# Kernel optimization log

Measured on AMD Instinct MI355X. Metric: run time of the kernel, lower is better.

Reference implementation:

```python
import jax, jax.numpy as jnp
import numpy as np

NUM_LEVELS = 4
RADIUS = 3


def bilinear_sample(feat, coords):
    """feat: (B,H,W,C); coords: (B, ..., 2) with [x,y] order. Returns (B, ..., C).
    Matches the original: corner indices are clipped FIRST, then weights are
    computed from the clipped indices."""
    B, H, W, C = feat.shape
    x = coords[..., 0]
    y = coords[..., 1]
    x0 = jnp.clip(jnp.floor(x).astype(jnp.int32), 0, W - 1)
    x1 = jnp.clip(jnp.floor(x).astype(jnp.int32) + 1, 0, W - 1)
    y0 = jnp.clip(jnp.floor(y).astype(jnp.int32), 0, H - 1)
    y1 = jnp.clip(jnp.floor(y).astype(jnp.int32) + 1, 0, H - 1)
    x0f = x0.astype(jnp.float32); x1f = x1.astype(jnp.float32)
    y0f = y0.astype(jnp.float32); y1f = y1.astype(jnp.float32)
    wa = (x1f - x) * (y1f - y)
    wb = (x1f - x) * (y - y0f)
    wc = (x - x0f) * (y1f - y)
    wd = (x - x0f) * (y - y0f)
    bidx = jnp.arange(B).reshape((B,) + (1,) * (coords.ndim - 2))
    Ia = feat[bidx, y0, x0]
    Ib = feat[bidx, y1, x0]
    Ic = feat[bidx, y0, x1]
    Id = feat[bidx, y1, x1]
    return wa[..., None] * Ia + wb[..., None] * Ib + wc[..., None] * Ic + wd[..., None] * Id


def _normalize(v):
    return v / (jnp.linalg.norm(v, axis=-1, keepdims=True) + 1e-06)


def setup_inputs() -> dict:
    key = jax.random.key(0)
    k1, k2, k3, k4 = jax.random.split(key, 4)
    B, H, W, C, N = 2, 64, 64, 256, 4096
    fmap1 = jax.random.normal(k1, (B, H, W, C), dtype=jnp.float32)
    fmap2 = jax.random.normal(k2, (B, H, W, C), dtype=jnp.float32)
    scale = jnp.array([W - 1, H - 1], dtype=jnp.float32)
    coords1 = jax.random.uniform(k3, (B, N, 2), dtype=jnp.float32) * scale
    coords2 = jax.random.uniform(k4, (B, N, 2), dtype=jnp.float32) * scale
    return {"fmap1": fmap1, "fmap2": fmap2, "coords1": coords1, "coords2": coords2}


def reference(fmap1, fmap2, coords1, coords2):
    r = RADIUS
    B, H, W, C = fmap1.shape
    feat1 = _normalize(bilinear_sample(fmap1, coords1))  # (B,N,C)
    # Offset grid, dy-major then dx (matches the original nested loops),
    # stored as [dx, dy] to match `coords + [dx, dy]`.
    d = jnp.arange(-r, r + 1, dtype=jnp.float32)
    dyg, dxg = jnp.meshgrid(d, d, indexing='ij')
    offs = jnp.stack([dxg.ravel(), dyg.ravel()], axis=-1)  # (K,2), K=(2r+1)^2
    corr_list = []
    fmap2_l = fmap2  # cascaded pyramid, as in the original
    for level in range(NUM_LEVELS):
        if level > 0:
            fmap2_l = jax.image.resize(
                fmap2_l, (B, H // 2 ** level, W // 2 ** level, C), method='bilinear')
        H_l, W_l = fmap2_l.shape[1], fmap2_l.shape[2]
        f2n = _normalize(fmap2_l)
        scale = 2.0 ** level
        c = coords2[:, :, None, :] / scale + offs[None, None, :, :]  # (B,N,K,2)
        c = jnp.clip(c, jnp.zeros(2, jnp.float32),
                     jnp.array([W_l - 1, H_l - 1], dtype=jnp.float32))
        feat2 = bilinear_sample(f2n, c)  # (B,N,K,C)
        corr_list.append(jnp.einsum('bnc,bnkc->bnk', feat1, feat2))
    return jnp.concatenate(corr_list, axis=-1)  # (B,N,NUM_LEVELS*K)
```

## Files before the change

### kernel.cpp

```cpp
#include <hip/hip_runtime.h>
#include <math.h>

#define NB   2
#define H0   64
#define W0   64
#define NC   256
#define NPTS 4096
#define NLVL 4
#define NK   49

__device__ __forceinline__ float wave_reduce_sum(float v) {
    for (int m = 32; m >= 1; m >>= 1)
        v += __shfl_xor(v, m, 64);
    return v;
}

__device__ __forceinline__ float wave_reduce_max(float v) {
    for (int m = 32; m >= 1; m >>= 1)
        v = fmaxf(v, __shfl_xor(v, m, 64));
    return v;
}

__device__ __forceinline__ int dot4i(unsigned a, unsigned b, int c) {
#if defined(__has_builtin)
#if __has_builtin(__builtin_amdgcn_sdot4)
    return __builtin_amdgcn_sdot4((int)a, (int)b, c, false);
#else
    c += (((int)(a << 24)) >> 24) * (((int)(b << 24)) >> 24);
    c += (((int)(a << 16)) >> 24) * (((int)(b << 16)) >> 24);
    c += (((int)(a <<  8)) >> 24) * (((int)(b <<  8)) >> 24);
    c += (((int)a) >> 24)         * (((int)b) >> 24);
    return c;
#endif
#else
    c += (((int)(a << 24)) >> 24) * (((int)(b << 24)) >> 24);
    c += (((int)(a << 16)) >> 24) * (((int)(b << 16)) >> 24);
    c += (((int)(a <<  8)) >> 24) * (((int)(b <<  8)) >> 24);
    c += (((int)a) >> 24)         * (((int)b) >> 24);
    return c;
#endif
}

__device__ __forceinline__ void quant_store(float nx, float ny, float nz, float nw,
                                            unsigned char* __restrict__ qout,
                                            size_t pixIdx,
                                            float* __restrict__ sout, int lane) {
    float m = fmaxf(fmaxf(fabsf(nx), fabsf(ny)), fmaxf(fabsf(nz), fabsf(nw)));
    float M = wave_reduce_max(m);
    float s = (M > 0.f) ? 127.f / M : 0.f;
    int qx = __float2int_rn(nx * s), qy = __float2int_rn(ny * s);
    int qz = __float2int_rn(nz * s), qw = __float2int_rn(nw * s);
    unsigned p = (qx & 0xff) | ((qy & 0xff) << 8) | ((qz & 0xff) << 16) | ((qw & 0xff) << 24);
    ((unsigned*)(qout + pixIdx * NC))[lane] = p;
    if (lane == 0) sout[pixIdx] = (M > 0.f) ? M / 127.f : 0.f;
}

__device__ __forceinline__ void down_norm(const float* __restrict__ in,
                                          float* __restrict__ raw_out,
                                          unsigned char* __restrict__ qout,
                                          float* __restrict__ sout,
                                          int Hi, int Wi, int wid, int lane) {
    int Ho = Hi >> 1, Wo = Wi >> 1;
    int b = wid / (Ho * Wo);
    int rem = wid - b * (Ho * Wo);
    int yo = rem / Wo, xo = rem - yo * Wo;
    float wy[4], wx[4]; int ty[4], tx[4];
    float sy = 0.f, sx = 0.f;
    for (int j = 0; j < 4; ++j) {
        float w = (j == 0 || j == 3) ? 1.f : 3.f;
        int yi = 2 * yo - 1 + j;
        float wyj = (yi >= 0 && yi < Hi) ? w : 0.f;
        ty[j] = min(max(yi, 0), Hi - 1); wy[j] = wyj; sy += wyj;
        int xi = 2 * xo - 1 + j;
        float wxj = (xi >= 0 && xi < Wi) ? w : 0.f;
        tx[j] = min(max(xi, 0), Wi - 1); wx[j] = wxj; sx += wxj;
    }
    float inv_s = 1.f / (sy * sx);
    float ax = 0.f, ay = 0.f, az = 0.f, aw = 0.f;
    const float4* basep = (const float4*)(in + (size_t)b * Hi * Wi * NC);
    for (int jy = 0; jy < 4; ++jy) {
        if (wy[jy] == 0.f) continue;
        for (int jx = 0; jx < 4; ++jx) {
            float w = wy[jy] * wx[jx];
            if (w == 0.f) continue;
            float4 v = basep[(ty[jy] * Wi + tx[jx]) * (NC / 4) + lane];
            ax += w * v.x; ay += w * v.y; az += w * v.z; aw += w * v.w;
        }
    }
    ax *= inv_s; ay *= inv_s; az *= inv_s; aw *= inv_s;
    float ss = wave_reduce_sum(ax * ax + ay * ay + az * az + aw * aw);
    float inv = 1.f / (sqrtf(ss) + 1e-6f);
    size_t po = (size_t)b * Ho * Wo + (size_t)yo * Wo + xo;
    if (raw_out) {
        float4 r; r.x = ax; r.y = ay; r.z = az; r.w = aw;
        ((float4*)raw_out)[po * (NC / 4) + lane] = r;
    }
    quant_store(ax * inv, ay * inv, az * inv, aw * inv, qout, po, sout, lane);
}

__global__ __launch_bounds__(256)
void pre_kernel(const float* __restrict__ fmap1,
                const float* __restrict__ fmap2,
                const float* __restrict__ coords1,
                unsigned char* __restrict__ f1q, float* __restrict__ fsc,
                unsigned char* __restrict__ q0,  float* __restrict__ s0,
                float* __restrict__ raw1,
                unsigned char* __restrict__ q1,  float* __restrict__ s1) {
    int blk  = blockIdx.x;
    int wv   = threadIdx.x >> 6;
    int lane = threadIdx.x & 63;
    if (blk < 2048) {
        int pt = blk * 4 + wv;
        int b = pt / NPTS;
        float x = coords1[pt * 2 + 0];
        float y = coords1[pt * 2 + 1];
        int x0 = min(max((int)floorf(x), 0), W0 - 1);
        int y0 = min(max((int)floorf(y), 0), H0 - 1);
        int x1 = min(x0 + 1, W0 - 1);
        int y1 = min(y0 + 1, H0 - 1);
        float wxh = x - (float)x0, wxl = (float)x1 - x;
        float wyh = y - (float)y0, wyl = (float)y1 - y;
        float wa = wxl * wyl, wb = wxl * wyh, wc = wxh * wyl, wd = wxh * wyh;
        const float4* base = (const float4*)(fmap1 + (size_t)b * H0 * W0 * NC);
        float4 Ia = base[(y0 * W0 + x0) * (NC / 4) + lane];
        float4 Ib = base[(y1 * W0 + x0) * (NC / 4) + lane];
        float4 Ic = base[(y0 * W0 + x1) * (NC / 4) + lane];
        float4 Id = base[(y1 * W0 + x1) * (NC / 4) + lane];
        float vx = wa * Ia.x + wb * Ib.x + wc * Ic.x + wd * Id.x;
        float vy = wa * Ia.y + wb * Ib.y + wc * Ic.y + wd * Id.y;
        float vz = wa * Ia.z + wb * Ib.z + wc * Ic.z + wd * Id.z;
        float vw = wa * Ia.w + wb * Ib.w + wc * Ic.w + wd * Id.w;
        float ss = wave_reduce_sum(vx * vx + vy * vy + vz * vz + vw * vw);
        float inv = 1.0f / (sqrtf(ss) + 1e-6f);
        quant_store(vx * inv, vy * inv, vz * inv, vw * inv, f1q, pt, fsc, lane);
    } else if (blk < 4096) {
        int p = (blk - 2048) * 4 + wv;
        float4 v = ((const float4*)fmap2)[(size_t)p * (NC / 4) + lane];
        float ss = wave_reduce_sum(v.x * v.x + v.y * v.y + v.z * v.z + v.w * v.w);
        float inv = 1.0f / (sqrtf(ss) + 1e-6f);
        quant_store(v.x * inv, v.y * inv, v.z * inv, v.w * inv, q0, p, s0, lane);
    } else {
        int wid = (blk - 4096) * 4 + wv;
        down_norm(fmap2, raw1, q1, s1, H0, W0, wid, lane);
    }
}

__global__ __launch_bounds__(256)
void small_kernel(const float* __restrict__ raw1,
                  unsigned char* __restrict__ q2, float* __restrict__ s2,
                  unsigned char* __restrict__ q3, float* __restrict__ s3) {
    __shared__ float4 part[4][64];
    int blk  = blockIdx.x;
    int wv   = threadIdx.x >> 6;
    int lane = threadIdx.x & 63;
    float ax = 0.f, ay = 0.f, az = 0.f, aw = 0.f;
    unsigned char* qout; float* sout; size_t po;

    if (blk < 512) {
        int b = blk >> 8, rem = blk & 255;
        int yo = rem >> 4, xo = rem & 15;
        float wy[4], wx[4]; int ty[4], tx[4];
        float sy = 0.f, sx = 0.f;
#pragma unroll
        for (int j = 0; j < 4; ++j) {
            float w = (j == 0 || j == 3) ? 1.f : 3.f;
            int yi = 2 * yo - 1 + j;
            float wyj = (yi >= 0 && yi < 32) ? w : 0.f;
            ty[j] = min(max(yi, 0), 31); wy[j] = wyj; sy += wyj;
            int xi = 2 * xo - 1 + j;
            float wxj = (xi >= 0 && xi < 32) ? w : 0.f;
            tx[j] = min(max(xi, 0), 31); wx[j] = wxj; sx += wxj;
        }
        float inv_s = 1.f / (sy * sx);
        const float4* basep = (const float4*)(raw1 + (size_t)b * 32 * 32 * NC);
        int jy = wv;
        if (wy[jy] != 0.f) {
#pragma unroll
            for (int jx = 0; jx < 4; ++jx) {
                float w = wy[jy] * wx[jx] * inv_s;
                if (wx[jx] == 0.f) continue;
                float4 v = basep[(ty[jy] * 32 + tx[jx]) * (NC / 4) + lane];
                ax += w * v.x; ay += w * v.y; az += w * v.z; aw += w * v.w;
            }
        }
        qout = q2; sout = s2; po = (size_t)b * 256 + yo * 16 + xo;
    } else {
        int wid = blk - 512;
        int b = wid >> 6, rem = wid & 63;
        int yo = rem >> 3, xo = rem & 7;
        float Wt[2][10]; int base[2];
        for (int d = 0; d < 2; ++d) {
            int o = d ? xo : yo;
            base[d] = 4 * o - 3;
            float W[10];
            for (int k = 0; k < 10; ++k) W[k] = 0.f;
            float S2 = 0.f;
            for (int j = 0; j < 4; ++j) {
                int yj = 2 * o - 1 + j;
                if (yj < 0 || yj >= 16) continue;
                float wj = (j == 0 || j == 3) ? 1.f : 3.f;
                S2 += wj;
                int yi0 = 2 * yj - 1;
                float wi[4], s1v = 0.f;
                for (int i2 = 0; i2 < 4; ++i2) {
                    int yi = yi0 + i2;
                    wi[i2] = (yi >= 0 && yi < 32) ? ((i2 == 0 || i2 == 3) ? 1.f : 3.f) : 0.f;
                    s1v += wi[i2];
                }
                float sc = wj / s1v;
                for (int i2 = 0; i2 < 4; ++i2)
                    if (wi[i2] > 0.f) W[yi0 + i2 - base[d]] += wi[i2] * sc;
            }
            float invS = 1.f / S2;
            for (int k = 0; k < 10; ++k) Wt[d][k] = W[k] * invS;
        }
        const float4* basep = (const float4*)(raw1 + (size_t)b * 32 * 32 * NC);
        for (int ky = wv; ky < 10; ky += 4) {
            float wyk = Wt[0][ky];
            if (wyk == 0.f) continue;
            int yi = base[0] + ky;
#pragma unroll
            for (int kx = 0; kx < 10; ++kx) {
                float wxk = Wt[1][kx];
                if (wxk == 0.f) continue;
                int xi = base[1] + kx;
                float wgt = wyk * wxk;
                float4 v = basep[(yi * 32 + xi) * (NC / 4) + lane];
                ax += wgt * v.x; ay += wgt * v.y; az += wgt * v.z; aw += wgt * v.w;
            }
        }
        qout = q3; sout = s3; po = (size_t)b * 64 + yo * 8 + xo;
    }

    float4 pr; pr.x = ax; pr.y = ay; pr.z = az; pr.w = aw;
    part[wv][lane] = pr;
    __syncthreads();
    if (wv == 0) {
        float4 p0 = part[0][lane], p1 = part[1][lane];
        float4 p2 = part[2][lane], p3 = part[3][lane];
        ax = p0.x + p1.x + p2.x + p3.x;
        ay = p0.y + p1.y + p2.y + p3.y;
        az = p0.z + p1.z + p2.z + p3.z;
        aw = p0.w + p1.w + p2.w + p3.w;
        float ss = wave_reduce_sum(ax * ax + ay * ay + az * az + aw * aw);
        float inv = 1.f / (sqrtf(ss) + 1e-6f);
        quant_store(ax * inv, ay * inv, az * inv, aw * inv, qout, po, sout, lane);
    }
}

__device__ __forceinline__ int tile_dot(const uint4* buf, const uint4* a4) {
    int ac = 0;
#pragma unroll
    for (int s = 0; s < 4; ++s) {
        uint4 u = buf[s], av = a4[s];
        ac = dot4i(av.x, u.x, ac);
        ac = dot4i(av.y, u.y, ac);
        ac = dot4i(av.z, u.z, ac);
        ac = dot4i(av.w, u.w, ac);
    }
    return ac;
}

__global__ __launch_bounds__(256)
void corr_kernel(const unsigned char* __restrict__ f1q,
                 const float* __restrict__ fsc,
                 const float* __restrict__ coords2,
                 const unsigned char* __restrict__ q0, const float* __restrict__ s0,
                 const unsigned char* __restrict__ q1, const float* __restrict__ s1,
                 const unsigned char* __restrict__ q2, const float* __restrict__ s2,
                 const unsigned char* __restrict__ q3, const float* __restrict__ s3,
                 float* __restrict__ out) {
    __shared__ float Ds[NLVL][64];
    int pt = blockIdx.x;
    int b  = pt / NPTS;
    int t  = threadIdx.x;

    int w    = t >> 6;
    int lane = t & 63;
    int Wl = W0 >> w, Hl = H0 >> w;
    float invs = 1.0f / (float)(1 << w);
    float cx = coords2[pt * 2 + 0] * invs;
    float cy = coords2[pt * 2 + 1] * invs;
    int ix = (int)floorf(cx), iy = (int)floorf(cy);

    const unsigned char* f2q = (w == 0) ? q0 : (w == 1) ? q1 : (w == 2) ? q2 : q3;
    const float*         f2s = (w == 0) ? s0 : (w == 1) ? s1 : (w == 2) ? s2 : s3;

    int cg = lane & 3;
    int pq = lane >> 2;

    const uint4* pixp[4];
    int pidx[4];
#pragma unroll
    for (int i = 0; i < 4; ++i) {
        int p  = i * 16 + pq;
        int jx = p & 7, jy = p >> 3;
        int px = min(max(ix - 3 + jx, 0), Wl - 1);
        int py = min(max(iy - 3 + jy, 0), Hl - 1);
        pidx[i] = (b * Hl + py) * Wl + px;
        pixp[i] = (const uint4*)(f2q + (size_t)pidx[i] * NC);
    }

    uint4 bufs[4][4];
#pragma unroll
    for (int i = 0; i < 4; ++i)
#pragma unroll
        for (int s = 0; s < 4; ++s)
            bufs[i][s] = pixp[i][s * 4 + cg];

    const uint4* f1p = (const uint4*)(f1q + (size_t)pt * NC);
    uint4 a4[4];
#pragma unroll
    for (int s = 0; s < 4; ++s) a4[s] = f1p[s * 4 + cg];

    float sb[4];
#pragma unroll
    for (int i = 0; i < 4; ++i) sb[i] = f2s[pidx[i]];
    float sa = fsc[pt];

#pragma unroll
    for (int i = 0; i < 4; ++i) {
        int r = tile_dot(bufs[i], a4);
        r += __shfl_xor(r, 1, 64);
        r += __shfl_xor(r, 2, 64);
        if (cg == 0) Ds[w][i * 16 + pq] = (float)r * sa * sb[i];
    }
    __syncthreads();

    if (lane < NK) {
        int tyk = lane / 7, txk = lane % 7;
        float dx = (float)(txk - 3), dy = (float)(tyk - 3);
        float x = fminf(fmaxf(cx + dx, 0.f), (float)(Wl - 1));
        float y = fminf(fmaxf(cy + dy, 0.f), (float)(Hl - 1));
        int x0 = (int)floorf(x);
        int y0 = (int)floorf(y);
        int x1 = min(x0 + 1, Wl - 1);
        int y1 = min(y0 + 1, Hl - 1);
        float wxh = x - (float)x0, wxl = (float)x1 - x;
        float wyh = y - (float)y0, wyl = (float)y1 - y;
        int sx0 = min(max(x0 - ix + 3, 0), 7);
        int sx1 = min(max(x1 - ix + 3, 0), 7);
        int sy0 = min(max(y0 - iy + 3, 0), 7);
        int sy1 = min(max(y1 - iy + 3, 0), 7);
        float v = wxl * wyl * Ds[w][sy0 * 8 + sx0]
                + wxl * wyh * Ds[w][sy1 * 8 + sx0]
                + wxh * wyl * Ds[w][sy0 * 8 + sx1]
                + wxh * wyh * Ds[w][sy1 * 8 + sx1];
        out[(size_t)pt * (NLVL * NK) + w * NK + lane] = v;
    }
}

extern "C" void kernel_launch(void* const* d_in, const int* in_sizes, int n_in,
                              void* d_out, int out_size, void* d_ws, size_t ws_size,
                              hipStream_t stream) {
    const float* fmap1   = (const float*)d_in[0];
    const float* fmap2   = (const float*)d_in[1];
    const float* coords1 = (const float*)d_in[2];
    const float* coords2 = (const float*)d_in[3];
    float* out = (float*)d_out;
    float* ws  = (float*)d_ws;

    float*         raw1 = ws;
    unsigned char* f1q  = (unsigned char*)(ws + 524288);
    float*         fsc  = ws + 1048576;
    unsigned char* q0   = (unsigned char*)(ws + 1056768);
    float*         s0   = ws + 1581056;
    unsigned char* q1   = (unsigned char*)(ws + 1589248);
    float*         s1   = ws + 1720320;
    unsigned char* q2   = (unsigned char*)(ws + 1722368);
    float*         s2   = ws + 1755136;
    unsigned char* q3   = (unsigned char*)(ws + 1755648);
    float*         s3   = ws + 1763840;

    pre_kernel<<<4608, 256, 0, stream>>>(fmap1, fmap2, coords1,
                                         f1q, fsc, q0, s0, raw1, q1, s1);
    small_kernel<<<640, 256, 0, stream>>>(raw1, q2, s2, q3, s3);
    corr_kernel<<<NB * NPTS, 256, 0, stream>>>(f1q, fsc, coords2,
                                               q0, s0, q1, s1, q2, s2, q3, s3, out);
}
```

Measured before the change: 109.6 us.

## Fuse pyramid build into one kernel by composing cascaded downsample weights

Removes the separate small_kernel launch and the full-precision level-1 intermediate buffer. Levels 2 and 3 are now computed straight from fmap2, using per-axis filter weights built by composing the cascaded 2x bilinear downsamples. This saves one launch and the write/read round trip of the raw level-1 map. In exchange, level-2/3 outputs read much wider footprints from the full-resolution map (up to about 22x22 pixels), and the weight arrays are dynamically indexed, which may spill to scratch. It also drops a block-wide barrier in corr_kernel, relying on each wave reading only its own shared slice.

```diff
diff --git a/kernel.cpp b/kernel.cpp
--- a/kernel.cpp
+++ b/kernel.cpp
@@ -56,7 +56,6 @@
 }
 
 __device__ __forceinline__ void down_norm(const float* __restrict__ in,
-                                          float* __restrict__ raw_out,
                                           unsigned char* __restrict__ qout,
                                           float* __restrict__ sout,
                                           int Hi, int Wi, int wid, int lane) {
@@ -91,21 +90,52 @@
     float ss = wave_reduce_sum(ax * ax + ay * ay + az * az + aw * aw);
     float inv = 1.f / (sqrtf(ss) + 1e-6f);
     size_t po = (size_t)b * Ho * Wo + (size_t)yo * Wo + xo;
-    if (raw_out) {
-        float4 r; r.x = ax; r.y = ay; r.z = az; r.w = aw;
-        ((float4*)raw_out)[po * (NC / 4) + lane] = r;
-    }
     quant_store(ax * inv, ay * inv, az * inv, aw * inv, qout, po, sout, lane);
 }
 
+__device__ void compose_axis(int o, int nst, float* W, int* pb0, int* pn) {
+    float a[22];
+    int ba = o, na = 1, ra = 64 >> nst;
+    a[0] = 1.f;
+    for (int s = 0; s < nst; ++s) {
+        float bt[22];
+        int rb = ra << 1;
+        int bb = 2 * ba - 1;
+        int nb = 2 * na + 2;
+        for (int k = 0; k < nb; ++k) bt[k] = 0.f;
+        for (int k = 0; k < na; ++k) {
+            float ak = a[k];
+            if (ak == 0.f) continue;
+            int j  = ba + k;
+            int i0 = 2 * j - 1;
+            float w0 = (i0     >= 0 && i0     < rb) ? 1.f : 0.f;
+            float w1 = (i0 + 1 >= 0 && i0 + 1 < rb) ? 3.f : 0.f;
+            float w2 = (i0 + 2 >= 0 && i0 + 2 < rb) ? 3.f : 0.f;
+            float w3 = (i0 + 3 >= 0 && i0 + 3 < rb) ? 1.f : 0.f;
+            float inv = ak / (w0 + w1 + w2 + w3);
+            int off = i0 - bb;
+            bt[off]     += w0 * inv;
+            bt[off + 1] += w1 * inv;
+            bt[off + 2] += w2 * inv;
+            bt[off + 3] += w3 * inv;
+        }
+        ba = bb; na = nb; ra = rb;
+        for (int k = 0; k < na; ++k) a[k] = bt[k];
+    }
+    *pb0 = ba; *pn = na;
+    for (int k = 0; k < na; ++k) W[k] = a[k];
+}
+
 __global__ __launch_bounds__(256)
-void pre_kernel(const float* __restrict__ fmap1,
-                const float* __restrict__ fmap2,
-                const float* __restrict__ coords1,
-                unsigned char* __restrict__ f1q, float* __restrict__ fsc,
-                unsigned char* __restrict__ q0,  float* __restrict__ s0,
-                float* __restrict__ raw1,
-                unsigned char* __restrict__ q1,  float* __restrict__ s1) {
+void build_kernel(const float* __restrict__ fmap1,
+                  const float* __restrict__ fmap2,
+                  const float* __restrict__ coords1,
+                  unsigned char* __restrict__ f1q, float* __restrict__ fsc,
+                  unsigned char* __restrict__ q0,  float* __restrict__ s0,
+                  unsigned char* __restrict__ q1,  float* __restrict__ s1,
+                  unsigned char* __restrict__ q2,  float* __restrict__ s2,
+                  unsigned char* __restrict__ q3,  float* __restrict__ s3) {
+    __shared__ float4 part[4][64];
     int blk  = blockIdx.x;
     int wv   = threadIdx.x >> 6;
     int lane = threadIdx.x & 63;
@@ -139,112 +169,55 @@
         float ss = wave_reduce_sum(v.x * v.x + v.y * v.y + v.z * v.z + v.w * v.w);
         float inv = 1.0f / (sqrtf(ss) + 1e-6f);
         quant_store(v.x * inv, v.y * inv, v.z * inv, v.w * inv, q0, p, s0, lane);
+    } else if (blk < 4608) {
+        int wid = (blk - 4096) * 4 + wv;
+        down_norm(fmap2, q1, s1, H0, W0, wid, lane);
     } else {
-        int wid = (blk - 4096) * 4 + wv;
-        down_norm(fmap2, raw1, q1, s1, H0, W0, wid, lane);
-    }
-}
-
-__global__ __launch_bounds__(256)
-void small_kernel(const float* __restrict__ raw1,
-                  unsigned char* __restrict__ q2, float* __restrict__ s2,
-                  unsigned char* __restrict__ q3, float* __restrict__ s3) {
-    __shared__ float4 part[4][64];
-    int blk  = blockIdx.x;
-    int wv   = threadIdx.x >> 6;
-    int lane = threadIdx.x & 63;
-    float ax = 0.f, ay = 0.f, az = 0.f, aw = 0.f;
-    unsigned char* qout; float* sout; size_t po;
-
-    if (blk < 512) {
-        int b = blk >> 8, rem = blk & 255;
-        int yo = rem >> 4, xo = rem & 15;
-        float wy[4], wx[4]; int ty[4], tx[4];
-        float sy = 0.f, sx = 0.f;
-#pragma unroll
-        for (int j = 0; j < 4; ++j) {
-            float w = (j == 0 || j == 3) ? 1.f : 3.f;
-            int yi = 2 * yo - 1 + j;
-            float wyj = (yi >= 0 && yi < 32) ? w : 0.f;
-            ty[j] = min(max(yi, 0), 31); wy[j] = wyj; sy += wyj;
-            int xi = 2 * xo - 1 + j;
-            float wxj = (xi >= 0 && xi < 32) ? w : 0.f;
-            tx[j] = min(max(xi, 0), 31); wx[j] = wxj; sx += wxj;
-        }
-        float inv_s = 1.f / (sy * sx);
-        const float4* basep = (const float4*)(raw1 + (size_t)b * 32 * 32 * NC);
-        int jy = wv;
-        if (wy[jy] != 0.f) {
-#pragma unroll
-            for (int jx = 0; jx < 4; ++jx) {
-                float w = wy[jy] * wx[jx] * inv_s;
-                if (wx[jx] == 0.f) continue;
-                float4 v = basep[(ty[jy] * 32 + tx[jx]) * (NC / 4) + lane];
+        int id = blk - 4608;
+        int b, yo, xo, nst;
+        unsigned char* qout; float* sout; size_t po;
+        if (id < 512) {
+            nst = 2;
+            b = id >> 8; int rem = id & 255; yo = rem >> 4; xo = rem & 15;
+            qout = q2; sout = s2; po = (size_t)b * 256 + yo * 16 + xo;
+        } else {
+            int id3 = id - 512;
+            nst = 3;
+            b = id3 >> 6; int rem = id3 & 63; yo = rem >> 3; xo = rem & 7;
+            qout = q3; sout = s3; po = (size_t)b * 64 + yo * 8 + xo;
+        }
+        float Wy[22], Wx[22];
+        int by, bx, ny, nx;
+        compose_axis(yo, nst, Wy, &by, &ny);
+        compose_axis(xo, nst, Wx, &bx, &nx);
+        const float4* basep = (const float4*)(fmap2 + (size_t)b * H0 * W0 * NC);
+        float ax = 0.f, ay = 0.f, az = 0.f, aw = 0.f;
+        for (int ky = wv; ky < ny; ky += 4) {
+            float wyk = Wy[ky];
+            if (wyk == 0.f) continue;
+            int yi = by + ky;
+            for (int kx = 0; kx < nx; ++kx) {
+                float wxk = Wx[kx];
+                if (wxk == 0.f) continue;
+                float w = wyk * wxk;
+                float4 v = basep[(yi * W0 + bx + kx) * (NC / 4) + lane];
                 ax += w * v.x; ay += w * v.y; az += w * v.z; aw += w * v.w;
             }
         }
-        qout = q2; sout = s2; po = (size_t)b * 256 + yo * 16 + xo;
-    } else {
-        int wid = blk - 512;
-        int b = wid >> 6, rem = wid & 63;
-        int yo = rem >> 3, xo = rem & 7;
-        float Wt[2][10]; int base[2];
-        for (int d = 0; d < 2; ++d) {
-            int o = d ? xo : yo;
-            base[d] = 4 * o - 3;
-            float W[10];
-            for (int k = 0; k < 10; ++k) W[k] = 0.f;
-            float S2 = 0.f;
-            for (int j = 0; j < 4; ++j) {
-                int yj = 2 * o - 1 + j;
-                if (yj < 0 || yj >= 16) continue;
-                float wj = (j == 0 || j == 3) ? 1.f : 3.f;
-                S2 += wj;
-                int yi0 = 2 * yj - 1;
-                float wi[4], s1v = 0.f;
-                for (int i2 = 0; i2 < 4; ++i2) {
-                    int yi = yi0 + i2;
-                    wi[i2] = (yi >= 0 && yi < 32) ? ((i2 == 0 || i2 == 3) ? 1.f : 3.f) : 0.f;
-                    s1v += wi[i2];
-                }
-                float sc = wj / s1v;
-                for (int i2 = 0; i2 < 4; ++i2)
-                    if (wi[i2] > 0.f) W[yi0 + i2 - base[d]] += wi[i2] * sc;
-            }
-            float invS = 1.f / S2;
-            for (int k = 0; k < 10; ++k) Wt[d][k] = W[k] * invS;
-        }
-        const float4* basep = (const float4*)(raw1 + (size_t)b * 32 * 32 * NC);
-        for (int ky = wv; ky < 10; ky += 4) {
-            float wyk = Wt[0][ky];
-            if (wyk == 0.f) continue;
-            int yi = base[0] + ky;
-#pragma unroll
-            for (int kx = 0; kx < 10; ++kx) {
-                float wxk = Wt[1][kx];
-                if (wxk == 0.f) continue;
-                int xi = base[1] + kx;
-                float wgt = wyk * wxk;
-                float4 v = basep[(yi * 32 + xi) * (NC / 4) + lane];
-                ax += wgt * v.x; ay += wgt * v.y; az += wgt * v.z; aw += wgt * v.w;
-            }
-        }
-        qout = q3; sout = s3; po = (size_t)b * 64 + yo * 8 + xo;
-    }
-
-    float4 pr; pr.x = ax; pr.y = ay; pr.z = az; pr.w = aw;
-    part[wv][lane] = pr;
-    __syncthreads();
-    if (wv == 0) {
-        float4 p0 = part[0][lane], p1 = part[1][lane];
-        float4 p2 = part[2][lane], p3 = part[3][lane];
-        ax = p0.x + p1.x + p2.x + p3.x;
-        ay = p0.y + p1.y + p2.y + p3.y;
-        az = p0.z + p1.z + p2.z + p3.z;
-        aw = p0.w + p1.w + p2.w + p3.w;
-        float ss = wave_reduce_sum(ax * ax + ay * ay + az * az + aw * aw);
-        float inv = 1.f / (sqrtf(ss) + 1e-6f);
-        quant_store(ax * inv, ay * inv, az * inv, aw * inv, qout, po, sout, lane);
+        float4 pr; pr.x = ax; pr.y = ay; pr.z = az; pr.w = aw;
+        part[wv][lane] = pr;
+        __syncthreads();
+        if (wv == 0) {
+            float4 p0 = part[0][lane], p1 = part[1][lane];
+            float4 p2 = part[2][lane], p3 = part[3][lane];
+            ax = p0.x + p1.x + p2.x + p3.x;
+            ay = p0.y + p1.y + p2.y + p3.y;
+            az = p0.z + p1.z + p2.z + p3.z;
+            aw = p0.w + p1.w + p2.w + p3.w;
+            float ss = wave_reduce_sum(ax * ax + ay * ay + az * az + aw * aw);
+            float inv = 1.f / (sqrtf(ss) + 1e-6f);
+            quant_store(ax * inv, ay * inv, az * inv, aw * inv, qout, po, sout, lane);
+        }
     }
 }
 
@@ -325,7 +298,6 @@
         r += __shfl_xor(r, 2, 64);
         if (cg == 0) Ds[w][i * 16 + pq] = (float)r * sa * sb[i];
     }
-    __syncthreads();
 
     if (lane < NK) {
         int tyk = lane / 7, txk = lane % 7;
@@ -360,21 +332,20 @@
     float* out = (float*)d_out;
     float* ws  = (float*)d_ws;
 
-    float*         raw1 = ws;
-    unsigned char* f1q  = (unsigned char*)(ws + 524288);
-    float*         fsc  = ws + 1048576;
-    unsigned char* q0   = (unsigned char*)(ws + 1056768);
-    float*         s0   = ws + 1581056;
-    unsigned char* q1   = (unsigned char*)(ws + 1589248);
-    float*         s1   = ws + 1720320;
-    unsigned char* q2   = (unsigned char*)(ws + 1722368);
-    float*         s2   = ws + 1755136;
-    unsigned char* q3   = (unsigned char*)(ws + 1755648);
-    float*         s3   = ws + 1763840;
-
-    pre_kernel<<<4608, 256, 0, stream>>>(fmap1, fmap2, coords1,
-                                         f1q, fsc, q0, s0, raw1, q1, s1);
-    small_kernel<<<640, 256, 0, stream>>>(raw1, q2, s2, q3, s3);
+    unsigned char* f1q = (unsigned char*)ws;
+    float*         fsc = ws + 524288;
+    unsigned char* q0  = (unsigned char*)(ws + 532480);
+    float*         s0  = ws + 1056768;
+    unsigned char* q1  = (unsigned char*)(ws + 1064960);
+    float*         s1  = ws + 1196032;
+    unsigned char* q2  = (unsigned char*)(ws + 1198080);
+    float*         s2  = ws + 1230848;
+    unsigned char* q3  = (unsigned char*)(ws + 1231360);
+    float*         s3  = ws + 1239552;
+
+    build_kernel<<<5248, 256, 0, stream>>>(fmap1, fmap2, coords1,
+                                           f1q, fsc, q0, s0, q1, s1,
+                                           q2, s2, q3, s3);
     corr_kernel<<<NB * NPTS, 256, 0, stream>>>(f1q, fsc, coords2,
                                                q0, s0, q1, s1, q2, s2, q3, s3, out);
 }
```

Result: slower. 162.4 us (+48.2%).
